# Kernel optimization log

Measured on AMD Instinct MI355X. Metric: run time of the kernel, lower is better.

Reference implementation:

```python
import jax, jax.numpy as jnp
import numpy as np

HEAD_SIZE = 64
BLOCK_SIZE = 4096
BATCH = 4


def setup_inputs() -> dict:
    key = jax.random.key(0)
    kx, kk, kq, kv = jax.random.split(key, 4)
    x = jax.random.normal(kx, (BATCH, BLOCK_SIZE, HEAD_SIZE), dtype=jnp.float32)
    s = HEAD_SIZE ** -0.5  # ~ torch default linear init scale
    Wk = jax.random.uniform(kk, (HEAD_SIZE, HEAD_SIZE), jnp.float32, -s, s)
    Wq = jax.random.uniform(kq, (HEAD_SIZE, HEAD_SIZE), jnp.float32, -s, s)
    Wv = jax.random.uniform(kv, (HEAD_SIZE, HEAD_SIZE), jnp.float32, -s, s)
    return {"x": x, "Wk": Wk, "Wq": Wq, "Wv": Wv}


def reference(x, Wk, Wq, Wv):
    # x: [B, T, C]; W*: [C, C] stored torch-style (out, in) -> y = x @ W.T
    B, T, C = x.shape
    k = x @ Wk.T  # [B, T, C]
    q = x @ Wq.T
    v = x @ Wv.T
    scores = jnp.einsum('btc,bsc->bts', q, k) * (C ** -0.5)  # [B, T, T]
    causal = jnp.tril(jnp.ones((T, T), dtype=bool))
    scores = jnp.where(causal, scores, -jnp.inf)
    weights = jax.nn.softmax(scores, axis=-1)
    out = jnp.einsum('bts,bsc->btc', weights, v)  # [B, T, C]
    return out
```

## Files before the change

### kernel.cpp

```cpp
#include <hip/hip_runtime.h>
#include <hip/hip_bf16.h>

typedef unsigned short u16;
typedef unsigned int u32;
typedef __bf16 bf16x8_t __attribute__((ext_vector_type(8)));
typedef float f32x4_t __attribute__((ext_vector_type(4)));

constexpr int Bb = 4;
constexpr int Tt = 4096;
constexpr int Dd = 64;
constexpr float QSCALE = 0.18033688011112042f;
constexpr int NSLOT = Bb * 128 * 16;

__device__ __forceinline__ u16 f2bf(float f) {
  unsigned int u = __builtin_bit_cast(unsigned int, f);
  return (u16)((u + 0x7fffu + ((u >> 16) & 1u)) >> 16);
}
__device__ __forceinline__ u32 pk2(float a, float b) {
  return (u32)f2bf(a) | ((u32)f2bf(b) << 16);
}
__device__ __forceinline__ u32 pkt(float a, float b) {
  const u32 ua = __builtin_bit_cast(u32, a);
  const u32 ub = __builtin_bit_cast(u32, b);
  return (ua >> 16) | (ub & 0xFFFF0000u);
}
__device__ __forceinline__ bf16x8_t ld16(const u16* p) {
  int4 v = *(const int4*)p;
  return __builtin_bit_cast(bf16x8_t, v);
}
__device__ __forceinline__ f32x4_t mfma16(bf16x8_t a, bf16x8_t b, f32x4_t c) {
  return __builtin_amdgcn_mfma_f32_16x16x32_bf16(a, b, c, 0, 0, 0);
}

__global__ __launch_bounds__(256) void HeadV1_proj(
    const float* __restrict__ x, const float* __restrict__ Wk,
    const float* __restrict__ Wq, const float* __restrict__ Wv,
    u16* __restrict__ qS, u16* __restrict__ kS, u16* __restrict__ vS)
{
  __shared__ u16 xl[64][72];
  __shared__ u16 Wl[3][64][72];
  __shared__ u16 ylds[64][72];

  const int t = threadIdx.x;
  const int w = t >> 6, lane = t & 63, l15 = lane & 15, quad = lane >> 4;
  const int r0 = blockIdx.x * 64;
  const int b  = r0 >> 12;
  const int kt = (r0 & 4095) >> 6;
  const long tilebase = ((long)(b * 64 + kt)) * 4096;

  {
    const float* srcs[4] = {x + (long)r0 * 64, Wk, Wq, Wv};
    u16* dstl[4] = {&xl[0][0], &Wl[0][0][0], &Wl[1][0][0], &Wl[2][0][0]};
    #pragma unroll
    for (int mm = 0; mm < 4; mm++) {
      const float* s = srcs[mm];
      u16* d = dstl[mm];
      #pragma unroll
      for (int i = 0; i < 4; i++) {
        const int f4 = i * 256 + t;
        const int row = f4 >> 4, c4 = f4 & 15;
        float4 v = ((const float4*)(s + row * 64))[c4];
        uint2 pk;
        pk.x = pk2(v.x, v.y);
        pk.y = pk2(v.z, v.w);
        *(uint2*)(d + row * 72 + c4 * 4) = pk;
      }
    }
  }
  __syncthreads();

  bf16x8_t xf[2];
  #pragma unroll
  for (int kh = 0; kh < 2; kh++)
    xf[kh] = ld16(&xl[w * 16 + l15][kh * 32 + quad * 8]);

  u16* dsts[3];
  dsts[0] = kS + tilebase; dsts[1] = qS + tilebase; dsts[2] = vS + tilebase;

  #pragma unroll
  for (int m = 0; m < 3; m++) {
    float vals[4][4];
    #pragma unroll
    for (int g = 0; g < 4; g++) {
      f32x4_t acc = {0.f, 0.f, 0.f, 0.f};
      #pragma unroll
      for (int kh = 0; kh < 2; kh++) {
        bf16x8_t wf = ld16(&Wl[m][g * 16 + l15][kh * 32 + quad * 8]);
        acc = mfma16(xf[kh], wf, acc);
      }
      #pragma unroll
      for (int r = 0; r < 4; r++)
        vals[g][r] = (m == 1) ? acc[r] * QSCALE : acc[r];
    }
    #pragma unroll
    for (int g = 0; g < 4; g++)
      #pragma unroll
      for (int r = 0; r < 4; r++)
        ylds[w * 16 + quad * 4 + r][g * 16 + l15] = f2bf(vals[g][r]);
    __syncthreads();
    if (m < 2) {
      #pragma unroll
      for (int kk = 0; kk < 2; kk++) {
        bf16x8_t f = ld16(&ylds[w * 16 + l15][kk * 32 + quad * 8]);
        *(int4*)(dsts[m] + (w * 2 + kk) * 512 + lane * 8) = __builtin_bit_cast(int4, f);
      }
    } else {
      #pragma unroll
      for (int kk = 0; kk < 2; kk++) {
        u16 tmp[8];
        #pragma unroll
        for (int j = 0; j < 8; j++)
          tmp[j] = ylds[kk * 32 + quad * 8 + j][w * 16 + l15];
        *(int4*)(dsts[2] + (kk * 4 + w) * 512 + lane * 8) = *(const int4*)tmp;
      }
    }
    __syncthreads();
  }
}

__global__ __launch_bounds__(64, 4) void HeadV1_part(
    const u16* __restrict__ qS, const u16* __restrict__ kS,
    const u16* __restrict__ vS, float* __restrict__ Opart,
    float* __restrict__ Lpart)
{
  __shared__ u16 pT[32][36];

  const int u = blockIdx.x;
  const int b = u & 3;
  const int j = (u >> 2) & 127;
  const int c = u >> 9;
  const int nk = (j >> 1) + 1;
  const int nc = (nk + 3) >> 2;
  if (c >= nc) return;

  const int lane = threadIdx.x;
  const int l15 = lane & 15, quad = lane >> 4;
  const int qt64 = j >> 1;
  const int ql0  = (j & 1) * 32;
  const int qr0  = j * 32;

  union { u32 u4[4]; bf16x8_t v; } uo;
  uo.u4[0] = uo.u4[1] = uo.u4[2] = uo.u4[3] = 0x3F803F80u;
  const bf16x8_t ones = uo.v;
  const f32x4_t zero4 = {0.f, 0.f, 0.f, 0.f};

  const u16* qtile = qS + ((long)(b * 64 + qt64)) * 4096 + lane * 8;
  bf16x8_t qfrag[2][2];
  #pragma unroll
  for (int ct = 0; ct < 2; ct++)
    #pragma unroll
    for (int kd = 0; kd < 2; kd++)
      qfrag[ct][kd] = ld16(qtile + ((ql0 / 16 + ct) * 2 + kd) * 512);

  f32x4_t O[4][2];
  #pragma unroll
  for (int a = 0; a < 4; a++)
    #pragma unroll
    for (int cc = 0; cc < 2; cc++)
      O[a][cc] = zero4;
  f32x4_t Lc[2] = {zero4, zero4};

  const int k0 = c * 4;
  const int kend = (k0 + 4 < nk) ? (k0 + 4) : nk;

  for (int kt = k0; kt < kend; ++kt) {
    const bool ismask = (kt == nk - 1);
    const int kv0 = kt * 64;
    const u16* ktile = kS + ((long)(b * 64 + kt)) * 4096 + lane * 8;
    const u16* vtile = vS + ((long)(b * 64 + kt)) * 4096 + lane * 8;

    #pragma unroll
    for (int kk = 0; kk < 2; kk++) {
      bf16x8_t vf[4];
      #pragma unroll
      for (int dt = 0; dt < 4; dt++)
        vf[dt] = ld16(vtile + (kk * 4 + dt) * 512);

      #pragma unroll
      for (int rtl = 0; rtl < 2; rtl++) {
        const int rt = kk * 2 + rtl;
        bf16x8_t kf0 = ld16(ktile + (rt * 2 + 0) * 512);
        bf16x8_t kf1 = ld16(ktile + (rt * 2 + 1) * 512);
        #pragma unroll
        for (int ct = 0; ct < 2; ct++) {
          f32x4_t acc = zero4;
          acc = mfma16(kf0, qfrag[ct][0], acc);
          acc = mfma16(kf1, qfrag[ct][1], acc);
          if (ismask) {
            const int kvl = kv0 + rt * 16 + quad * 4;
            const int qi  = qr0 + ct * 16 + l15;
            #pragma unroll
            for (int r = 0; r < 4; r++)
              if (kvl + r > qi) acc[r] = -1e30f;
          }
          const float p0 = __builtin_amdgcn_exp2f(acc[0]);
          const float p1 = __builtin_amdgcn_exp2f(acc[1]);
          const float p2 = __builtin_amdgcn_exp2f(acc[2]);
          const float p3 = __builtin_amdgcn_exp2f(acc[3]);
          uint2 pk;
          pk.x = pkt(p0, p1);
          pk.y = pkt(p2, p3);
          *(uint2*)&pT[ct * 16 + l15][rtl * 16 + quad * 4] = pk;
        }
      }
      #pragma unroll
      for (int ct = 0; ct < 2; ct++) {
        bf16x8_t pf = ld16(&pT[ct * 16 + l15][quad * 8]);
        #pragma unroll
        for (int dt = 0; dt < 4; dt++)
          O[dt][ct] = mfma16(vf[dt], pf, O[dt][ct]);
        Lc[ct] = mfma16(ones, pf, Lc[ct]);
      }
    }
  }

  const long slot = (long)((b * 128 + j) * 16 + c);
  float* Op = Opart + slot * 2048;
  #pragma unroll
  for (int dt = 0; dt < 4; dt++)
    #pragma unroll
    for (int ct = 0; ct < 2; ct++)
      *(f32x4_t*)(Op + ((dt * 2 + ct) * 64 + lane) * 4) = O[dt][ct];
  if (quad == 0) {
    Lpart[slot * 32 + l15]      = Lc[0][0];
    Lpart[slot * 32 + 16 + l15] = Lc[1][0];
  }
}

__global__ __launch_bounds__(256) void HeadV1_merge(
    const float* __restrict__ Opart, const float* __restrict__ Lpart,
    float* __restrict__ outg)
{
  __shared__ float Ls[32];
  const int t = threadIdx.x;
  const int lane = t & 63, w = t >> 6;
  const int b = blockIdx.x & 3;
  const int j = blockIdx.x >> 2;
  const int nk = (j >> 1) + 1;
  const int nc = (nk + 3) >> 2;
  const long slotbase = (long)((b * 128 + j) * 16);

  f32x4_t a0 = {0.f, 0.f, 0.f, 0.f}, a1 = {0.f, 0.f, 0.f, 0.f};
  for (int c = 0; c < nc; ++c) {
    const float* Op = Opart + (slotbase + c) * 2048;
    a0 += *(const f32x4_t*)(Op + (w * 64 + lane) * 4);
    a1 += *(const f32x4_t*)(Op + ((w + 4) * 64 + lane) * 4);
  }
  if (t < 32) {
    float s = 0.f;
    for (int c = 0; c < nc; ++c) s += Lpart[(slotbase + c) * 32 + t];
    Ls[t] = s;
  }
  __syncthreads();

  const int ct = w & 1, dtA = w >> 1, dtB = dtA + 2;
  const int q = ct * 16 + (lane & 15);
  const int d0 = (lane >> 4) * 4;
  const float invL = 1.0f / Ls[q];
  float* outp = outg + ((long)b * Tt + (long)j * 32 + q) * Dd;
  f32x4_t vA = a0 * invL;
  f32x4_t vB = a1 * invL;
  *(f32x4_t*)(outp + dtA * 16 + d0) = vA;
  *(f32x4_t*)(outp + dtB * 16 + d0) = vB;
}

extern "C" void kernel_launch(void* const* d_in, const int* in_sizes, int n_in,
                              void* d_out, int out_size, void* d_ws, size_t ws_size,
                              hipStream_t stream) {
  (void)in_sizes; (void)n_in; (void)out_size; (void)ws_size;
  const float* x  = (const float*)d_in[0];
  const float* Wk = (const float*)d_in[1];
  const float* Wq = (const float*)d_in[2];
  const float* Wv = (const float*)d_in[3];
  float* out = (float*)d_out;
  u16* qw = (u16*)d_ws;
  u16* kw = qw + (size_t)Bb * Tt * Dd;
  u16* vw = kw + (size_t)Bb * Tt * Dd;
  float* Op = (float*)(vw + (size_t)Bb * Tt * Dd);
  float* Lp = Op + (size_t)NSLOT * 2048;

  HeadV1_proj<<<(Bb * Tt) / 64, 256, 0, stream>>>(x, Wk, Wq, Wv, qw, kw, vw);
  HeadV1_part<<<NSLOT, 64, 0, stream>>>(qw, kw, vw, Op, Lp);
  HeadV1_merge<<<Bb * 128, 256, 0, stream>>>(Op, Lp, out);
}
```

Measured before the change: 100.1 us.

## Share K/V tiles in LDS across 8 query-row waves with double buffering

Replaces the single-wave partial-attention kernel (one block per query strip and KV chunk) with 512-thread blocks where 8 waves handle 8 adjacent 32-row query strips. They share K/V tiles staged in double-buffered LDS, with the next tile prefetched into registers. KV ranges are split across blocks with a precomputed group/chunk table so causal work is balanced. This cuts redundant global K/V reads. The cost is only 256 blocks, block-wide barriers each tile, and wasted iterations for waves whose causal range ends earlier.

```diff
diff --git a/kernel.cpp b/kernel.cpp
--- a/kernel.cpp
+++ b/kernel.cpp
@@ -10,7 +10,6 @@
 constexpr int Tt = 4096;
 constexpr int Dd = 64;
 constexpr float QSCALE = 0.18033688011112042f;
-constexpr int NSLOT = Bb * 128 * 16;
 
 __device__ __forceinline__ u16 f2bf(float f) {
   unsigned int u = __builtin_bit_cast(unsigned int, f);
@@ -118,23 +117,31 @@
   }
 }
 
-__global__ __launch_bounds__(64, 4) void HeadV1_part(
+__global__ __launch_bounds__(512) void HeadV1_flash(
     const u16* __restrict__ qS, const u16* __restrict__ kS,
     const u16* __restrict__ vS, float* __restrict__ Opart,
     float* __restrict__ Lpart)
 {
-  __shared__ u16 pT[32][36];
-
-  const int u = blockIdx.x;
-  const int b = u & 3;
-  const int j = (u >> 2) & 127;
-  const int c = u >> 9;
-  const int nk = (j >> 1) + 1;
-  const int nc = (nk + 3) >> 2;
-  if (c >= nc) return;
-
-  const int lane = threadIdx.x;
-  const int l15 = lane & 15, quad = lane >> 4;
+  __shared__ u16 kl[2][4096];
+  __shared__ u16 vl[2][4096];
+  __shared__ u16 pT[8][32][36];
+
+  const int t = threadIdx.x;
+  const int w = t >> 6, lane = t & 63, l15 = lane & 15, quad = lane >> 4;
+  const int b  = blockIdx.x & 3;
+  const int sb = blockIdx.x >> 2;
+
+  constexpr int PRE[17] = {0,1,2,4,6,8,11,14,18,22,27,32,38,44,50,57,64};
+  int g = 0, c = 0, n = 1;
+  #pragma unroll
+  for (int gg = 0; gg < 16; gg++)
+    if (sb >= PRE[gg] && sb < PRE[gg + 1]) { g = gg; c = sb - PRE[gg]; n = PRE[gg + 1] - PRE[gg]; }
+  const int R  = 4 * g + 4;
+  const int k0 = (R * c) / n;
+  const int k1 = (R * (c + 1)) / n;
+
+  const int j    = 8 * g + w;
+  const int nk   = (j >> 1) + 1;
   const int qt64 = j >> 1;
   const int ql0  = (j & 1) * 32;
   const int qr0  = j * 32;
@@ -160,61 +167,85 @@
       O[a][cc] = zero4;
   f32x4_t Lc[2] = {zero4, zero4};
 
-  const int k0 = c * 4;
-  const int kend = (k0 + 4 < nk) ? (k0 + 4) : nk;
-
-  for (int kt = k0; kt < kend; ++kt) {
-    const bool ismask = (kt == nk - 1);
-    const int kv0 = kt * 64;
-    const u16* ktile = kS + ((long)(b * 64 + kt)) * 4096 + lane * 8;
-    const u16* vtile = vS + ((long)(b * 64 + kt)) * 4096 + lane * 8;
-
-    #pragma unroll
-    for (int kk = 0; kk < 2; kk++) {
-      bf16x8_t vf[4];
-      #pragma unroll
-      for (int dt = 0; dt < 4; dt++)
-        vf[dt] = ld16(vtile + (kk * 4 + dt) * 512);
-
-      #pragma unroll
-      for (int rtl = 0; rtl < 2; rtl++) {
-        const int rt = kk * 2 + rtl;
-        bf16x8_t kf0 = ld16(ktile + (rt * 2 + 0) * 512);
-        bf16x8_t kf1 = ld16(ktile + (rt * 2 + 1) * 512);
+  {
+    const long tb = ((long)(b * 64 + k0)) * 4096 + t * 8;
+    int4 kr = *(const int4*)(kS + tb);
+    int4 vr = *(const int4*)(vS + tb);
+    *(int4*)&kl[0][t * 8] = kr;
+    *(int4*)&vl[0][t * 8] = vr;
+  }
+  __syncthreads();
+
+  for (int kt = k0; kt < k1; ++kt) {
+    const int cur = (kt - k0) & 1;
+    const bool more = (kt + 1 < k1);
+    int4 krn, vrn;
+    if (more) {
+      const long tb = ((long)(b * 64 + kt + 1)) * 4096 + t * 8;
+      krn = *(const int4*)(kS + tb);
+      vrn = *(const int4*)(vS + tb);
+    }
+
+    if (kt < nk) {
+      const bool ismask = (kt == nk - 1);
+      const int kv0 = kt * 64;
+      const u16* ktileL = &kl[cur][lane * 8];
+      const u16* vtileL = &vl[cur][lane * 8];
+
+      #pragma unroll
+      for (int kk = 0; kk < 2; kk++) {
+        bf16x8_t vf[4];
+        #pragma unroll
+        for (int dt = 0; dt < 4; dt++)
+          vf[dt] = ld16(vtileL + (kk * 4 + dt) * 512);
+
+        #pragma unroll
+        for (int rtl = 0; rtl < 2; rtl++) {
+          const int rt = kk * 2 + rtl;
+          bf16x8_t kf0 = ld16(ktileL + (rt * 2 + 0) * 512);
+          bf16x8_t kf1 = ld16(ktileL + (rt * 2 + 1) * 512);
+          #pragma unroll
+          for (int ct = 0; ct < 2; ct++) {
+            f32x4_t acc = zero4;
+            acc = mfma16(kf0, qfrag[ct][0], acc);
+            acc = mfma16(kf1, qfrag[ct][1], acc);
+            if (ismask) {
+              const int kvl = kv0 + rt * 16 + quad * 4;
+              const int qi  = qr0 + ct * 16 + l15;
+              #pragma unroll
+              for (int r = 0; r < 4; r++)
+                if (kvl + r > qi) acc[r] = -1e30f;
+            }
+            const float p0 = __builtin_amdgcn_exp2f(acc[0]);
+            const float p1 = __builtin_amdgcn_exp2f(acc[1]);
+            const float p2 = __builtin_amdgcn_exp2f(acc[2]);
+            const float p3 = __builtin_amdgcn_exp2f(acc[3]);
+            uint2 pk;
+            pk.x = pkt(p0, p1);
+            pk.y = pkt(p2, p3);
+            *(uint2*)&pT[w][ct * 16 + l15][rtl * 16 + quad * 4] = pk;
+          }
+        }
         #pragma unroll
         for (int ct = 0; ct < 2; ct++) {
-          f32x4_t acc = zero4;
-          acc = mfma16(kf0, qfrag[ct][0], acc);
-          acc = mfma16(kf1, qfrag[ct][1], acc);
-          if (ismask) {
-            const int kvl = kv0 + rt * 16 + quad * 4;
-            const int qi  = qr0 + ct * 16 + l15;
-            #pragma unroll
-            for (int r = 0; r < 4; r++)
-              if (kvl + r > qi) acc[r] = -1e30f;
-          }
-          const float p0 = __builtin_amdgcn_exp2f(acc[0]);
-          const float p1 = __builtin_amdgcn_exp2f(acc[1]);
-          const float p2 = __builtin_amdgcn_exp2f(acc[2]);
-          const float p3 = __builtin_amdgcn_exp2f(acc[3]);
-          uint2 pk;
-          pk.x = pkt(p0, p1);
-          pk.y = pkt(p2, p3);
-          *(uint2*)&pT[ct * 16 + l15][rtl * 16 + quad * 4] = pk;
+          bf16x8_t pf = ld16(&pT[w][ct * 16 + l15][quad * 8]);
+          #pragma unroll
+          for (int dt = 0; dt < 4; dt++)
+            O[dt][ct] = mfma16(vf[dt], pf, O[dt][ct]);
+          Lc[ct] = mfma16(ones, pf, Lc[ct]);
         }
       }
-      #pragma unroll
-      for (int ct = 0; ct < 2; ct++) {
-        bf16x8_t pf = ld16(&pT[ct * 16 + l15][quad * 8]);
-        #pragma unroll
-        for (int dt = 0; dt < 4; dt++)
-          O[dt][ct] = mfma16(vf[dt], pf, O[dt][ct]);
-        Lc[ct] = mfma16(ones, pf, Lc[ct]);
-      }
-    }
-  }
-
-  const long slot = (long)((b * 128 + j) * 16 + c);
+    }
+
+    if (more) {
+      __syncthreads();
+      *(int4*)&kl[cur ^ 1][t * 8] = krn;
+      *(int4*)&vl[cur ^ 1][t * 8] = vrn;
+      __syncthreads();
+    }
+  }
+
+  const long slot = (long)((b * 128 + j) * 8 + c);
   float* Op = Opart + slot * 2048;
   #pragma unroll
   for (int dt = 0; dt < 4; dt++)
@@ -236,9 +267,12 @@
   const int lane = t & 63, w = t >> 6;
   const int b = blockIdx.x & 3;
   const int j = blockIdx.x >> 2;
-  const int nk = (j >> 1) + 1;
-  const int nc = (nk + 3) >> 2;
-  const long slotbase = (long)((b * 128 + j) * 16);
+  constexpr int NCHK[16] = {1,1,2,2,2,3,3,4,4,5,5,6,6,6,7,7};
+  int nc = 1;
+  #pragma unroll
+  for (int gg = 0; gg < 16; gg++)
+    if ((j >> 3) == gg) nc = NCHK[gg];
+  const long slotbase = (long)((b * 128 + j) * 8);
 
   f32x4_t a0 = {0.f, 0.f, 0.f, 0.f}, a1 = {0.f, 0.f, 0.f, 0.f};
   for (int c = 0; c < nc; ++c) {
@@ -277,9 +311,9 @@
   u16* kw = qw + (size_t)Bb * Tt * Dd;
   u16* vw = kw + (size_t)Bb * Tt * Dd;
   float* Op = (float*)(vw + (size_t)Bb * Tt * Dd);
-  float* Lp = Op + (size_t)NSLOT * 2048;
+  float* Lp = Op + (size_t)(Bb * 128 * 8) * 2048;
 
   HeadV1_proj<<<(Bb * Tt) / 64, 256, 0, stream>>>(x, Wk, Wq, Wv, qw, kw, vw);
-  HeadV1_part<<<NSLOT, 64, 0, stream>>>(qw, kw, vw, Op, Lp);
+  HeadV1_flash<<<256, 512, 0, stream>>>(qw, kw, vw, Op, Lp);
   HeadV1_merge<<<Bb * 128, 256, 0, stream>>>(Op, Lp, out);
 }
```

After: 100.7 us. No clear change (+0.5%).
